# Optimization experiments

Measured on AMD Instinct MI355X. Metric: run time of the kernel, lower is better.

## Reference

```python
import jax, jax.numpy as jnp
import numpy as np

D_MODEL = 1024
N_HEADS = 16
HEAD_DIM = D_MODEL // N_HEADS
ROPE_BASE = 10000.0
RMS_EPS = 1e-5


def setup_inputs() -> dict:
    key = jax.random.key(0)
    k1, k2, k3 = jax.random.split(key, 3)
    B, T = 2, 2048
    x = jax.random.normal(k1, (B, T, D_MODEL), dtype=jnp.float32)
    norm_w = jnp.ones((D_MODEL,), dtype=jnp.float32)
    w_qkv = jax.random.normal(k2, (3 * D_MODEL, D_MODEL), dtype=jnp.float32) * (D_MODEL ** -0.5)
    w_out = jax.random.normal(k3, (D_MODEL, D_MODEL), dtype=jnp.float32) * (D_MODEL ** -0.5)
    return {"x": x, "norm_w": norm_w, "w_qkv": w_qkv, "w_out": w_out}


def _rope_cos_sin(T, dtype):
    inv_freq = 1.0 / (ROPE_BASE ** (jnp.arange(0, HEAD_DIM, 2, dtype=jnp.float32) / HEAD_DIM))
    t = jnp.arange(T, dtype=jnp.float32)
    freqs = t[:, None] * inv_freq[None, :]            # [T, HEAD_DIM//2]
    emb = jnp.concatenate([freqs, freqs], axis=-1)    # [T, HEAD_DIM]
    return jnp.cos(emb).astype(dtype), jnp.sin(emb).astype(dtype)


def _rotate_half(x):
    x1, x2 = jnp.split(x, 2, axis=-1)
    return jnp.concatenate([-x2, x1], axis=-1)


def reference(x, norm_w, w_qkv, w_out):
    B, T, _ = x.shape
    residual = x
    # RMSNorm
    rms = jax.lax.rsqrt(jnp.mean(x * x, axis=-1, keepdims=True) + RMS_EPS)
    xn = x * rms * norm_w
    # QKV projection (torch Linear: x @ W.T)
    qkv = xn @ w_qkv.T                                  # [B, T, 3*D]
    qkv = qkv.reshape(B, T, 3, N_HEADS, HEAD_DIM)
    q, k, v = qkv[:, :, 0], qkv[:, :, 1], qkv[:, :, 2]  # [B, T, H, hd]
    # RoPE on q, k
    cos, sin = _rope_cos_sin(T, q.dtype)                # [T, hd]
    cos = cos[None, :, None, :]
    sin = sin[None, :, None, :]
    q = q * cos + _rotate_half(q) * sin
    k = k * cos + _rotate_half(k) * sin
    # Bidirectional SDPA: [B, H, T, hd]
    qh = q.transpose(0, 2, 1, 3)
    kh = k.transpose(0, 2, 1, 3)
    vh = v.transpose(0, 2, 1, 3)
    scale = HEAD_DIM ** -0.5
    scores = jnp.einsum('bhqd,bhkd->bhqk', qh, kh) * scale
    attn = jax.nn.softmax(scores, axis=-1)
    out = jnp.einsum('bhqk,bhkd->bhqd', attn, vh)       # [B, H, T, hd]
    out = out.transpose(0, 2, 1, 3).reshape(B, T, D_MODEL)
    out = out @ w_out.T
    return residual + out
```

## Files before the change

kernel.cpp:

```cpp
#include <hip/hip_runtime.h>
#include <hip/hip_bf16.h>
#include <math.h>


typedef __bf16 bf16;
typedef __bf16 bf16x8 __attribute__((ext_vector_type(8)));
typedef __bf16 bf16x4 __attribute__((ext_vector_type(4)));
typedef float  f32x4  __attribute__((ext_vector_type(4)));
typedef unsigned u32x4 __attribute__((ext_vector_type(4)));

#define GLOAD16(g, l) __builtin_amdgcn_global_load_lds( \
    (const __attribute__((address_space(1))) void*)(g),  \
    (__attribute__((address_space(3))) void*)(l), 16, 0, 0)

__device__ __forceinline__ unsigned pk2(float a, float b) {
  unsigned short lo = __builtin_bit_cast(unsigned short, (bf16)a);
  unsigned short hi = __builtin_bit_cast(unsigned short, (bf16)b);
  return (unsigned)lo | ((unsigned)hi << 16);
}

__global__ __launch_bounds__(256) void k_cvt(const float* __restrict__ src,
    bf16* __restrict__ dst, int n) {
  int i = (blockIdx.x * 256 + threadIdx.x) * 8;
  if (i >= n) return;
  float4 a = *(const float4*)(src + i);
  float4 b = *(const float4*)(src + i + 4);
  bf16x8 o;
  o[0] = (bf16)a.x; o[1] = (bf16)a.y; o[2] = (bf16)a.z; o[3] = (bf16)a.w;
  o[4] = (bf16)b.x; o[5] = (bf16)b.y; o[6] = (bf16)b.z; o[7] = (bf16)b.w;
  *(bf16x8*)(dst + i) = o;
}

__global__ __launch_bounds__(256) void k_tab(float2* __restrict__ tab) {
  int idx = blockIdx.x * 256 + threadIdx.x;
  int t = idx >> 5, j = idx & 31;
  float invf = exp2f(-0.41524101186f * (float)j);
  float th = (float)t * invf;
  float sn, cs;
  sincosf(th, &sn, &cs);
  tab[idx] = make_float2(cs, sn);
}

__global__ __launch_bounds__(256) void k_rmsnorm(const float* __restrict__ x,
    const float* __restrict__ w, bf16* __restrict__ xn) {
  const int row = blockIdx.x, tid = threadIdx.x;
  float4 v = *(const float4*)(x + (size_t)row * 1024 + tid * 4);
  float ss = v.x * v.x + v.y * v.y + v.z * v.z + v.w * v.w;
  for (int m = 32; m >= 1; m >>= 1) ss += __shfl_xor(ss, m);
  __shared__ float red[4];
  if ((tid & 63) == 0) red[tid >> 6] = ss;
  __syncthreads();
  float ms = (red[0] + red[1] + red[2] + red[3]) * (1.f / 1024.f);
  float r = rsqrtf(ms + 1e-5f);
  float4 wv = *(const float4*)(w + tid * 4);
  bf16x4 o;
  o[0] = (bf16)(v.x * r * wv.x); o[1] = (bf16)(v.y * r * wv.y);
  o[2] = (bf16)(v.z * r * wv.z); o[3] = (bf16)(v.w * r * wv.w);
  *(bf16x4*)(xn + (size_t)row * 1024 + tid * 4) = o;
}

template<int RESID, int TM, int ROPE>
__global__ __launch_bounds__(256, (TM == 128) ? 3 : 2) void k_gemm_bt(
    const bf16* __restrict__ A, const bf16* __restrict__ B,
    const float* __restrict__ R, void* __restrict__ Cv,
    int M, int N, int K, int lda, const float2* __restrict__ tab) {
  constexpr int MT = TM / 32;
  constexpr int AELEM = TM * 64;
  constexpr int SMEM = (AELEM + 8192 > TM * 136) ? (AELEM + 8192) : (TM * 136);
  const int tid = threadIdx.x;
  const int lane = tid & 63, L15 = lane & 15, quad = lane >> 4;
  const int wave = tid >> 6, wr = wave >> 1, wc = wave & 1;
  const int n0 = blockIdx.x * 128, m0 = blockIdx.y * TM;
  __shared__ __align__(16) bf16 smem[SMEM];
  bf16* sA = smem; bf16* sB = smem + AELEM;
  f32x4 acc[MT][4];
  const f32x4 z = {0.f, 0.f, 0.f, 0.f};
  for (int i = 0; i < MT; i++) for (int j = 0; j < 4; j++) acc[i][j] = z;

  for (int k0 = 0; k0 < K; k0 += 64) {
    const bf16* Ab = A + (size_t)m0 * lda + k0;
    const bf16* Bb = B + (size_t)n0 * K + k0;
    for (int p = 0; p < TM / 32; p++) {
      int s = p * 256 + tid, r = s >> 3, c8 = (s & 7) ^ (r & 7);
      GLOAD16(Ab + (size_t)r * lda + c8 * 8, sA + s * 8);
    }
    for (int p = 0; p < 4; p++) {
      int s = p * 256 + tid, r = s >> 3, c8 = (s & 7) ^ (r & 7);
      GLOAD16(Bb + (size_t)r * K + c8 * 8, sB + s * 8);
    }
    __syncthreads();
    for (int kk = 0; kk < 2; kk++) {
      bf16x8 af[MT], bfv[4];
      for (int i = 0; i < MT; i++) {
        int ra = wr * (TM / 2) + i * 16 + L15;
        af[i] = *(const bf16x8*)(sA + ra * 64 + (((kk * 4 + quad) ^ (ra & 7)) * 8));
      }
      for (int i = 0; i < 4; i++) {
        int rb = wc * 64 + i * 16 + L15;
        bfv[i] = *(const bf16x8*)(sB + rb * 64 + (((kk * 4 + quad) ^ (rb & 7)) * 8));
      }
      __builtin_amdgcn_s_setprio(1);
      for (int mt = 0; mt < MT; mt++)
        for (int nt = 0; nt < 4; nt++)
          acc[mt][nt] = __builtin_amdgcn_mfma_f32_16x16x32_bf16(af[mt], bfv[nt], acc[mt][nt], 0, 0, 0);
      __builtin_amdgcn_s_setprio(0);
    }
    __syncthreads();
  }
  if (ROPE && (n0 >> 10) < 2) {
    const float qs = ((n0 >> 10) == 0) ? 0.18033688011f : 1.0f;
    const int tb = (m0 & 2047) + wr * (TM / 2);
    for (int mt = 0; mt < MT; mt++) {
      for (int nt = 0; nt < 2; nt++) {
        const int j = nt * 16 + L15;
        for (int g = 0; g < 4; g++) {
          int t = tb + mt * 16 + quad * 4 + g;
          float2 cs = tab[t * 32 + j];
          float lo = acc[mt][nt][g], hi = acc[mt][nt + 2][g];
          acc[mt][nt][g]     = (lo * cs.x - hi * cs.y) * qs;
          acc[mt][nt + 2][g] = (hi * cs.x + lo * cs.y) * qs;
        }
      }
    }
  }
  bf16* sC = smem;
  for (int mt = 0; mt < MT; mt++) for (int nt = 0; nt < 4; nt++) {
    int r = wr * (TM / 2) + mt * 16 + quad * 4, c = wc * 64 + nt * 16 + L15;
    f32x4 v = acc[mt][nt];
    for (int g = 0; g < 4; g++) sC[(r + g) * 136 + c] = (bf16)v[g];
  }
  __syncthreads();
  constexpr int TPR = 256 / TM;
  constexpr int CPT = 128 / TPR;
  const int rr = tid / TPR, sg = (tid % TPR) * CPT;
  const size_t row = (size_t)m0 + rr;
  const bf16* src = sC + rr * 136 + sg;
  if (RESID) {
    float* Cf = (float*)Cv;
    const float* rs = R + row * N + n0 + sg;
    float* dst = Cf + row * N + n0 + sg;
    for (int i = 0; i < CPT / 4; i++) {
      bf16x4 u = *(const bf16x4*)(src + i * 4);
      float4 rv = *(const float4*)(rs + i * 4);
      float4 o;
      o.x = (float)u[0] + rv.x; o.y = (float)u[1] + rv.y;
      o.z = (float)u[2] + rv.z; o.w = (float)u[3] + rv.w;
      *(float4*)(dst + i * 4) = o;
    }
  } else {
    bf16* Cb = (bf16*)Cv;
    bf16* dst = Cb + row * N + n0 + sg;
    for (int i = 0; i < CPT / 8; i++)
      *(bf16x8*)(dst + i * 8) = *(const bf16x8*)(src + i * 8);
  }
}

__global__ __launch_bounds__(256) void k_vt(const bf16* __restrict__ qkv,
    bf16* __restrict__ vt) {
  const int blk = blockIdx.x;
  const int tt = blk & 31, h = (blk >> 5) & 15, b = blk >> 9;
  const int tid = threadIdx.x;
  const int bh = b * 16 + h;
  __shared__ __align__(16) bf16 sT[64 * 72];
  for (int p = 0; p < 2; p++) {
    int s = p * 256 + tid, tl = s >> 3, c = s & 7;
    const bf16* vsrc = qkv + (size_t)(b * 2048 + tt * 64 + tl) * 3072 + 2048 + h * 64 + c * 8;
    *(bf16x8*)(sT + tl * 72 + c * 8) = *(const bf16x8*)vsrc;
  }
  __syncthreads();
  for (int p = 0; p < 2; p++) {
    int s = p * 256 + tid, d = s >> 3, tc = s & 7;
    bf16x8 v;
    for (int j = 0; j < 8; j++) v[j] = sT[(tc * 8 + j) * 72 + d];
    *(bf16x8*)(vt + (size_t)bh * 131072 + (size_t)d * 2048 + tt * 64 + tc * 8) = v;
  }
}

__global__ __launch_bounds__(256, 2) void k_attn(bf16* __restrict__ qkv,
    const bf16* __restrict__ vt) {
  const int tid = threadIdx.x;
  const int lane = tid & 63, L15 = lane & 15, quad = lane >> 4;
  const int wave = tid >> 6;
  const int bh = blockIdx.y, b = bh >> 4, h = bh & 15;
  const int q0 = blockIdx.x * 128;
  const bf16* Q  = qkv + (size_t)b * 2048 * 3072 + h * 64;
  const bf16* Kg = qkv + (size_t)b * 2048 * 3072 + 1024 + h * 64;
  const bf16* Vg = vt + (size_t)bh * 131072;
  __shared__ __align__(16) bf16 smem[32768];

  bf16x8 qf[2][2];
  for (int qt = 0; qt < 2; qt++) for (int kk = 0; kk < 2; kk++) {
    int rq = q0 + wave * 32 + qt * 16 + L15;
    qf[qt][kk] = *(const bf16x8*)(Q + (size_t)rq * 3072 + kk * 32 + quad * 8);
  }
  f32x4 o[4][2];
  const f32x4 z = {0.f, 0.f, 0.f, 0.f};
  for (int i = 0; i < 4; i++) for (int j = 0; j < 2; j++) o[i][j] = z;
  f32x4 o5[2] = {z, z};
  const bf16 one = (bf16)1.0f;
  const bf16x8 ones8 = {one, one, one, one, one, one, one, one};
  const float mcl = 7.21347602f;
  const f32x4 minit = {-mcl, -mcl, -mcl, -mcl};

  auto STAGE = [&](int kv0, int base) {
    const bf16* Kb = Kg + (size_t)kv0 * 3072;
    bf16* sKb = smem + base;
    bf16* sVb = smem + base + 8192;
    for (int p = 0; p < 4; p++) {
      int s = p * 256 + tid, r = s >> 3, c8 = (s & 7) ^ (r & 7);
      GLOAD16(Kb + (size_t)r * 3072 + c8 * 8, sKb + s * 8);
    }
    for (int p = 0; p < 4; p++) {
      int s = p * 256 + tid, r = s >> 4, cl = s & 15;
      int c8 = (cl & 8) | ((cl ^ (r & 7)) & 7);
      GLOAD16(Vg + (size_t)r * 2048 + kv0 + c8 * 8, sVb + s * 8);
    }
  };

  STAGE(0, 0);
  for (int t = 0; t < 16; ++t) {
    const int cur = (t & 1) << 14;
    if (t < 15) {
      STAGE((t + 1) << 7, cur ^ 16384);
      asm volatile("s_waitcnt vmcnt(8)" ::: "memory");
    } else {
      asm volatile("s_waitcnt vmcnt(0)" ::: "memory");
    }
    __builtin_amdgcn_s_barrier();
    __builtin_amdgcn_sched_barrier(0);
    const bf16* sK = smem + cur;
    const bf16* sV = smem + cur + 8192;

    f32x4 st[8][2];
    {
      bf16x8 kf[8];
#pragma unroll
      for (int kvt = 0; kvt < 8; kvt++) {
        int rk = kvt * 16 + L15;
        kf[kvt] = *(const bf16x8*)(sK + rk * 64 + ((quad ^ (rk & 7)) * 8));
      }
      __builtin_amdgcn_s_setprio(1);
#pragma unroll
      for (int kvt = 0; kvt < 8; kvt++)
        for (int qt = 0; qt < 2; qt++)
          st[kvt][qt] = __builtin_amdgcn_mfma_f32_16x16x32_bf16(kf[kvt], qf[qt][0], minit, 0, 0, 0);
      __builtin_amdgcn_s_setprio(0);
    }
    {
      bf16x8 kf[8];
#pragma unroll
      for (int kvt = 0; kvt < 8; kvt++) {
        int rk = kvt * 16 + L15;
        kf[kvt] = *(const bf16x8*)(sK + rk * 64 + (((4 + quad) ^ (rk & 7)) * 8));
      }
      __builtin_amdgcn_s_setprio(1);
#pragma unroll
      for (int kvt = 0; kvt < 8; kvt++)
        for (int qt = 0; qt < 2; qt++)
          st[kvt][qt] = __builtin_amdgcn_mfma_f32_16x16x32_bf16(kf[kvt], qf[qt][1], st[kvt][qt], 0, 0, 0);
      __builtin_amdgcn_s_setprio(0);
    }
    unsigned pA[2][8], pB[2][8];
#pragma unroll
    for (int qt = 0; qt < 2; qt++)
      for (int kvt = 0; kvt < 8; kvt++) {
        float p0 = __builtin_amdgcn_exp2f(st[kvt][qt][0]);
        float p1 = __builtin_amdgcn_exp2f(st[kvt][qt][1]);
        float p2 = __builtin_amdgcn_exp2f(st[kvt][qt][2]);
        float p3 = __builtin_amdgcn_exp2f(st[kvt][qt][3]);
        pA[qt][kvt] = pk2(p0, p1);
        pB[qt][kvt] = pk2(p2, p3);
      }
#pragma unroll
    for (int kc = 0; kc < 4; kc++) {
      bf16x8 vf[4];
#pragma unroll
      for (int dt = 0; dt < 4; dt++) {
        int rd = dt * 16 + L15;
        int c = kc * 4 + quad;
        int cs = (c & 8) | ((c ^ (rd & 7)) & 7);
        vf[dt] = *(const bf16x8*)(sV + rd * 128 + cs * 8);
      }
#pragma unroll
      for (int qt = 0; qt < 2; qt++) {
        auto rA = __builtin_amdgcn_permlane32_swap(pA[qt][2 * kc], pA[qt][2 * kc + 1], false, false);
        auto tAC = __builtin_amdgcn_permlane16_swap(rA[0], rA[1], false, false);
        auto rB = __builtin_amdgcn_permlane32_swap(pB[qt][2 * kc], pB[qt][2 * kc + 1], false, false);
        auto tBD = __builtin_amdgcn_permlane16_swap(rB[0], rB[1], false, false);
        u32x4 pw;
        pw[0] = tAC[0]; pw[1] = tBD[0]; pw[2] = tAC[1]; pw[3] = tBD[1];
        bf16x8 pf = __builtin_bit_cast(bf16x8, pw);
        __builtin_amdgcn_s_setprio(1);
#pragma unroll
        for (int dt = 0; dt < 4; dt++)
          o[dt][qt] = __builtin_amdgcn_mfma_f32_16x16x32_bf16(vf[dt], pf, o[dt][qt], 0, 0, 0);
        o5[qt] = __builtin_amdgcn_mfma_f32_16x16x32_bf16(ones8, pf, o5[qt], 0, 0, 0);
        __builtin_amdgcn_s_setprio(0);
      }
    }
    asm volatile("s_waitcnt lgkmcnt(0)" ::: "memory");
    __builtin_amdgcn_sched_barrier(0);
    __builtin_amdgcn_s_barrier();
  }
  float invl[2] = {1.f / o5[0][0], 1.f / o5[1][0]};
  bf16* sO = smem;
  for (int dt = 0; dt < 4; dt++) for (int qt = 0; qt < 2; qt++) {
    f32x4 v = o[dt][qt] * invl[qt];
    int ql = wave * 32 + qt * 16 + L15;
    uint2 w2; w2.x = pk2(v[0], v[1]); w2.y = pk2(v[2], v[3]);
    *(uint2*)(sO + ql * 72 + dt * 16 + quad * 4) = w2;
  }
  __syncthreads();
  const int rr = tid >> 1, sg = (tid & 1) * 32;
  const bf16* src = sO + rr * 72 + sg;
  bf16* dst = qkv + (size_t)(b * 2048 + q0 + rr) * 3072 + h * 64 + sg;
  for (int i = 0; i < 4; i++)
    *(bf16x8*)(dst + i * 8) = *(const bf16x8*)(src + i * 8);
}

extern "C" void kernel_launch(void* const* d_in, const int* in_sizes, int n_in,
                              void* d_out, int out_size, void* d_ws, size_t ws_size,
                              hipStream_t stream) {
  (void)in_sizes; (void)n_in; (void)out_size;
  const float* x     = (const float*)d_in[0];
  const float* normw = (const float*)d_in[1];
  const float* wqkv  = (const float*)d_in[2];
  const float* wout  = (const float*)d_in[3];
  float* out = (float*)d_out;
  bf16* ws  = (bf16*)d_ws;
  const size_t NQKV = (size_t)4096 * 3072, NXN = (size_t)4096 * 1024;
  const size_t NWQ = (size_t)3072 * 1024, NWO = (size_t)1024 * 1024;
  const size_t need = (NQKV + NXN + NWQ + NWO) * sizeof(bf16);
  if (ws_size < need) return;
  bf16* qkv    = ws;
  bf16* xn     = qkv + NQKV;
  bf16* vtp    = xn;
  bf16* wqkvb  = xn + NXN;
  bf16* woutb  = wqkvb + NWQ;
  float2* tab  = (float2*)out;
  k_cvt<<<(int)(NWQ / 8 / 256), 256, 0, stream>>>(wqkv, wqkvb, (int)NWQ);
  k_cvt<<<(int)(NWO / 8 / 256), 256, 0, stream>>>(wout, woutb, (int)NWO);
  k_tab<<<256, 256, 0, stream>>>(tab);
  k_rmsnorm<<<4096, 256, 0, stream>>>(x, normw, xn);
  k_gemm_bt<0, 128, 1><<<dim3(24, 32), 256, 0, stream>>>(xn, wqkvb, nullptr, qkv, 4096, 3072, 1024, 1024, tab);
  k_vt<<<1024, 256, 0, stream>>>(qkv, vtp);
  k_attn<<<dim3(16, 32), 256, 0, stream>>>(qkv, vtp);
  k_gemm_bt<1, 64, 0><<<dim3(8, 64), 256, 0, stream>>>(qkv, woutb, x, out, 4096, 1024, 1024, 3072, nullptr);
}
```

Baseline: 202.7 us.

## Split attention KV tile across two wave groups with shared-memory reduction

The attention kernel now runs 512 threads per block. Two groups of four waves each handle half of every 128-key tile for the same 128 queries, and the partial outputs and row sums are combined through shared memory at the end. The goal is more waves per block and less serial work per wave, which should improve latency hiding. The cost is an extra reduction step with shared-memory traffic and barriers, plus higher register and occupancy pressure from the 512,4 launch bounds.

Result: slower. 207.9 us (+2.6%).

```diff
diff --git a/kernel.cpp b/kernel.cpp
--- a/kernel.cpp
+++ b/kernel.cpp
@@ -176,11 +176,13 @@
   }
 }
 
-__global__ __launch_bounds__(256, 2) void k_attn(bf16* __restrict__ qkv,
+__global__ __launch_bounds__(512, 4) void k_attn(bf16* __restrict__ qkv,
     const bf16* __restrict__ vt) {
   const int tid = threadIdx.x;
   const int lane = tid & 63, L15 = lane & 15, quad = lane >> 4;
   const int wave = tid >> 6;
+  const int qw = wave & 3;
+  const int kvh = wave >> 2;
   const int bh = blockIdx.y, b = bh >> 4, h = bh & 15;
   const int q0 = blockIdx.x * 128;
   const bf16* Q  = qkv + (size_t)b * 2048 * 3072 + h * 64;
@@ -190,7 +192,7 @@
 
   bf16x8 qf[2][2];
   for (int qt = 0; qt < 2; qt++) for (int kk = 0; kk < 2; kk++) {
-    int rq = q0 + wave * 32 + qt * 16 + L15;
+    int rq = q0 + qw * 32 + qt * 16 + L15;
     qf[qt][kk] = *(const bf16x8*)(Q + (size_t)rq * 3072 + kk * 32 + quad * 8);
   }
   f32x4 o[4][2];
@@ -206,12 +208,12 @@
     const bf16* Kb = Kg + (size_t)kv0 * 3072;
     bf16* sKb = smem + base;
     bf16* sVb = smem + base + 8192;
-    for (int p = 0; p < 4; p++) {
-      int s = p * 256 + tid, r = s >> 3, c8 = (s & 7) ^ (r & 7);
+    for (int p = 0; p < 2; p++) {
+      int s = p * 512 + tid, r = s >> 3, c8 = (s & 7) ^ (r & 7);
       GLOAD16(Kb + (size_t)r * 3072 + c8 * 8, sKb + s * 8);
     }
-    for (int p = 0; p < 4; p++) {
-      int s = p * 256 + tid, r = s >> 4, cl = s & 15;
+    for (int p = 0; p < 2; p++) {
+      int s = p * 512 + tid, r = s >> 4, cl = s & 15;
       int c8 = (cl & 8) | ((cl ^ (r & 7)) & 7);
       GLOAD16(Vg + (size_t)r * 2048 + kv0 + c8 * 8, sVb + s * 8);
     }
@@ -222,7 +224,7 @@
     const int cur = (t & 1) << 14;
     if (t < 15) {
       STAGE((t + 1) << 7, cur ^ 16384);
-      asm volatile("s_waitcnt vmcnt(8)" ::: "memory");
+      asm volatile("s_waitcnt vmcnt(4)" ::: "memory");
     } else {
       asm volatile("s_waitcnt vmcnt(0)" ::: "memory");
     }
@@ -231,39 +233,39 @@
     const bf16* sK = smem + cur;
     const bf16* sV = smem + cur + 8192;
 
-    f32x4 st[8][2];
+    f32x4 st[4][2];
     {
-      bf16x8 kf[8];
-#pragma unroll
-      for (int kvt = 0; kvt < 8; kvt++) {
-        int rk = kvt * 16 + L15;
+      bf16x8 kf[4];
+#pragma unroll
+      for (int kvt = 0; kvt < 4; kvt++) {
+        int rk = kvh * 64 + kvt * 16 + L15;
         kf[kvt] = *(const bf16x8*)(sK + rk * 64 + ((quad ^ (rk & 7)) * 8));
       }
       __builtin_amdgcn_s_setprio(1);
 #pragma unroll
-      for (int kvt = 0; kvt < 8; kvt++)
+      for (int kvt = 0; kvt < 4; kvt++)
         for (int qt = 0; qt < 2; qt++)
           st[kvt][qt] = __builtin_amdgcn_mfma_f32_16x16x32_bf16(kf[kvt], qf[qt][0], minit, 0, 0, 0);
       __builtin_amdgcn_s_setprio(0);
     }
     {
-      bf16x8 kf[8];
-#pragma unroll
-      for (int kvt = 0; kvt < 8; kvt++) {
-        int rk = kvt * 16 + L15;
+      bf16x8 kf[4];
+#pragma unroll
+      for (int kvt = 0; kvt < 4; kvt++) {
+        int rk = kvh * 64 + kvt * 16 + L15;
         kf[kvt] = *(const bf16x8*)(sK + rk * 64 + (((4 + quad) ^ (rk & 7)) * 8));
       }
       __builtin_amdgcn_s_setprio(1);
 #pragma unroll
-      for (int kvt = 0; kvt < 8; kvt++)
+      for (int kvt = 0; kvt < 4; kvt++)
         for (int qt = 0; qt < 2; qt++)
           st[kvt][qt] = __builtin_amdgcn_mfma_f32_16x16x32_bf16(kf[kvt], qf[qt][1], st[kvt][qt], 0, 0, 0);
       __builtin_amdgcn_s_setprio(0);
     }
-    unsigned pA[2][8], pB[2][8];
+    unsigned pA[2][4], pB[2][4];
 #pragma unroll
     for (int qt = 0; qt < 2; qt++)
-      for (int kvt = 0; kvt < 8; kvt++) {
+      for (int kvt = 0; kvt < 4; kvt++) {
         float p0 = __builtin_amdgcn_exp2f(st[kvt][qt][0]);
         float p1 = __builtin_amdgcn_exp2f(st[kvt][qt][1]);
         float p2 = __builtin_amdgcn_exp2f(st[kvt][qt][2]);
@@ -272,12 +274,12 @@
         pB[qt][kvt] = pk2(p2, p3);
       }
 #pragma unroll
-    for (int kc = 0; kc < 4; kc++) {
+    for (int kc = 0; kc < 2; kc++) {
       bf16x8 vf[4];
 #pragma unroll
       for (int dt = 0; dt < 4; dt++) {
         int rd = dt * 16 + L15;
-        int c = kc * 4 + quad;
+        int c = kvh * 8 + kc * 4 + quad;
         int cs = (c & 8) | ((c ^ (rd & 7)) & 7);
         vf[dt] = *(const bf16x8*)(sV + rd * 128 + cs * 8);
       }
@@ -302,19 +304,36 @@
     __builtin_amdgcn_sched_barrier(0);
     __builtin_amdgcn_s_barrier();
   }
-  float invl[2] = {1.f / o5[0][0], 1.f / o5[1][0]};
-  bf16* sO = smem;
-  for (int dt = 0; dt < 4; dt++) for (int qt = 0; qt < 2; qt++) {
-    f32x4 v = o[dt][qt] * invl[qt];
-    int ql = wave * 32 + qt * 16 + L15;
-    uint2 w2; w2.x = pk2(v[0], v[1]); w2.y = pk2(v[2], v[3]);
-    *(uint2*)(sO + ql * 72 + dt * 16 + quad * 4) = w2;
-  }
-  __syncthreads();
-  const int rr = tid >> 1, sg = (tid & 1) * 32;
+  float* pO = (float*)smem;
+  float* pL = (float*)smem + 8704;
+  if (kvh == 1) {
+    for (int dt = 0; dt < 4; dt++) for (int qt = 0; qt < 2; qt++) {
+      int ql = qw * 32 + qt * 16 + L15;
+      *(f32x4*)(pO + (size_t)ql * 68 + dt * 16 + quad * 4) = o[dt][qt];
+    }
+    if (quad == 0)
+      for (int qt = 0; qt < 2; qt++)
+        pL[qw * 32 + qt * 16 + L15] = o5[qt][0];
+  }
+  __syncthreads();
+  bf16* sO = smem + 18432;
+  if (kvh == 0) {
+    float invl[2];
+    for (int qt = 0; qt < 2; qt++)
+      invl[qt] = 1.f / (o5[qt][0] + pL[qw * 32 + qt * 16 + L15]);
+    for (int dt = 0; dt < 4; dt++) for (int qt = 0; qt < 2; qt++) {
+      int ql = qw * 32 + qt * 16 + L15;
+      f32x4 part = *(const f32x4*)(pO + (size_t)ql * 68 + dt * 16 + quad * 4);
+      f32x4 v = (o[dt][qt] + part) * invl[qt];
+      uint2 w2; w2.x = pk2(v[0], v[1]); w2.y = pk2(v[2], v[3]);
+      *(uint2*)(sO + ql * 72 + dt * 16 + quad * 4) = w2;
+    }
+  }
+  __syncthreads();
+  const int rr = tid >> 2, sg = (tid & 3) * 16;
   const bf16* src = sO + rr * 72 + sg;
   bf16* dst = qkv + (size_t)(b * 2048 + q0 + rr) * 3072 + h * 64 + sg;
-  for (int i = 0; i < 4; i++)
+  for (int i = 0; i < 2; i++)
     *(bf16x8*)(dst + i * 8) = *(const bf16x8*)(src + i * 8);
 }
 
@@ -344,6 +363,6 @@
   k_rmsnorm<<<4096, 256, 0, stream>>>(x, normw, xn);
   k_gemm_bt<0, 128, 1><<<dim3(24, 32), 256, 0, stream>>>(xn, wqkvb, nullptr, qkv, 4096, 3072, 1024, 1024, tab);
   k_vt<<<1024, 256, 0, stream>>>(qkv, vtp);
-  k_attn<<<dim3(16, 32), 256, 0, stream>>>(qkv, vtp);
+  k_attn<<<dim3(16, 32), 512, 0, stream>>>(qkv, vtp);
   k_gemm_bt<1, 64, 0><<<dim3(8, 64), 256, 0, stream>>>(qkv, woutb, x, out, 4096, 1024, 1024, 3072, nullptr);
 }
```

## Merge prep kernels into one launch and interleave softmax exp with PV MFMAs

Applied to the files above, without the earlier changes.

Four preprocessing launches (two weight conversions, the RoPE table and RMSNorm) become a single k_prep kernel that picks its task by block index, removing three launch gaps. In the attention inner loop, the exp2 and bf16 packing of scores now happen per kc chunk, just before each group of PV MFMAs, instead of for the whole tile up front. This lowers the number of packed registers held at once and lets the exp work interleave with the MFMAs. The cost is more branching in the prep kernel and heavier reliance on the compiler's scheduling.

Measured after the change: 200.5 us. About the same (-1.1%).

```diff
diff --git a/kernel.cpp b/kernel.cpp
--- a/kernel.cpp
+++ b/kernel.cpp
@@ -19,31 +19,35 @@
   return (unsigned)lo | ((unsigned)hi << 16);
 }
 
-__global__ __launch_bounds__(256) void k_cvt(const float* __restrict__ src,
-    bf16* __restrict__ dst, int n) {
-  int i = (blockIdx.x * 256 + threadIdx.x) * 8;
-  if (i >= n) return;
-  float4 a = *(const float4*)(src + i);
-  float4 b = *(const float4*)(src + i + 4);
-  bf16x8 o;
-  o[0] = (bf16)a.x; o[1] = (bf16)a.y; o[2] = (bf16)a.z; o[3] = (bf16)a.w;
-  o[4] = (bf16)b.x; o[5] = (bf16)b.y; o[6] = (bf16)b.z; o[7] = (bf16)b.w;
-  *(bf16x8*)(dst + i) = o;
-}
-
-__global__ __launch_bounds__(256) void k_tab(float2* __restrict__ tab) {
-  int idx = blockIdx.x * 256 + threadIdx.x;
-  int t = idx >> 5, j = idx & 31;
-  float invf = exp2f(-0.41524101186f * (float)j);
-  float th = (float)t * invf;
-  float sn, cs;
-  sincosf(th, &sn, &cs);
-  tab[idx] = make_float2(cs, sn);
-}
-
-__global__ __launch_bounds__(256) void k_rmsnorm(const float* __restrict__ x,
-    const float* __restrict__ w, bf16* __restrict__ xn) {
-  const int row = blockIdx.x, tid = threadIdx.x;
+__global__ __launch_bounds__(256) void k_prep(
+    const float* __restrict__ wqkv, const float* __restrict__ wout,
+    const float* __restrict__ x, const float* __restrict__ w,
+    bf16* __restrict__ wqkvb, bf16* __restrict__ woutb,
+    bf16* __restrict__ xn, float2* __restrict__ tab) {
+  const int bid = blockIdx.x, tid = threadIdx.x;
+  if (bid < 2048) {
+    const float* src = (bid < 1536) ? wqkv : wout;
+    bf16* dst = (bid < 1536) ? wqkvb : woutb;
+    int i = ((bid < 1536 ? bid : bid - 1536) * 256 + tid) * 8;
+    float4 a = *(const float4*)(src + i);
+    float4 b = *(const float4*)(src + i + 4);
+    bf16x8 o;
+    o[0] = (bf16)a.x; o[1] = (bf16)a.y; o[2] = (bf16)a.z; o[3] = (bf16)a.w;
+    o[4] = (bf16)b.x; o[5] = (bf16)b.y; o[6] = (bf16)b.z; o[7] = (bf16)b.w;
+    *(bf16x8*)(dst + i) = o;
+    return;
+  }
+  if (bid < 2304) {
+    int idx = (bid - 2048) * 256 + tid;
+    int t = idx >> 5, j = idx & 31;
+    float invf = exp2f(-0.41524101186f * (float)j);
+    float th = (float)t * invf;
+    float sn, cs;
+    sincosf(th, &sn, &cs);
+    tab[idx] = make_float2(cs, sn);
+    return;
+  }
+  const int row = bid - 2304;
   float4 v = *(const float4*)(x + (size_t)row * 1024 + tid * 4);
   float ss = v.x * v.x + v.y * v.y + v.z * v.z + v.w * v.w;
   for (int m = 32; m >= 1; m >>= 1) ss += __shfl_xor(ss, m);
@@ -260,17 +264,6 @@
           st[kvt][qt] = __builtin_amdgcn_mfma_f32_16x16x32_bf16(kf[kvt], qf[qt][1], st[kvt][qt], 0, 0, 0);
       __builtin_amdgcn_s_setprio(0);
     }
-    unsigned pA[2][8], pB[2][8];
-#pragma unroll
-    for (int qt = 0; qt < 2; qt++)
-      for (int kvt = 0; kvt < 8; kvt++) {
-        float p0 = __builtin_amdgcn_exp2f(st[kvt][qt][0]);
-        float p1 = __builtin_amdgcn_exp2f(st[kvt][qt][1]);
-        float p2 = __builtin_amdgcn_exp2f(st[kvt][qt][2]);
-        float p3 = __builtin_amdgcn_exp2f(st[kvt][qt][3]);
-        pA[qt][kvt] = pk2(p0, p1);
-        pB[qt][kvt] = pk2(p2, p3);
-      }
 #pragma unroll
     for (int kc = 0; kc < 4; kc++) {
       bf16x8 vf[4];
@@ -281,11 +274,23 @@
         int cs = (c & 8) | ((c ^ (rd & 7)) & 7);
         vf[dt] = *(const bf16x8*)(sV + rd * 128 + cs * 8);
       }
+      unsigned pA[2][2], pB[2][2];
+#pragma unroll
+      for (int qt = 0; qt < 2; qt++)
+        for (int kq = 0; kq < 2; kq++) {
+          const f32x4 s4 = st[2 * kc + kq][qt];
+          float p0 = __builtin_amdgcn_exp2f(s4[0]);
+          float p1 = __builtin_amdgcn_exp2f(s4[1]);
+          float p2 = __builtin_amdgcn_exp2f(s4[2]);
+          float p3 = __builtin_amdgcn_exp2f(s4[3]);
+          pA[qt][kq] = pk2(p0, p1);
+          pB[qt][kq] = pk2(p2, p3);
+        }
 #pragma unroll
       for (int qt = 0; qt < 2; qt++) {
-        auto rA = __builtin_amdgcn_permlane32_swap(pA[qt][2 * kc], pA[qt][2 * kc + 1], false, false);
+        auto rA = __builtin_amdgcn_permlane32_swap(pA[qt][0], pA[qt][1], false, false);
         auto tAC = __builtin_amdgcn_permlane16_swap(rA[0], rA[1], false, false);
-        auto rB = __builtin_amdgcn_permlane32_swap(pB[qt][2 * kc], pB[qt][2 * kc + 1], false, false);
+        auto rB = __builtin_amdgcn_permlane32_swap(pB[qt][0], pB[qt][1], false, false);
         auto tBD = __builtin_amdgcn_permlane16_swap(rB[0], rB[1], false, false);
         u32x4 pw;
         pw[0] = tAC[0]; pw[1] = tBD[0]; pw[2] = tAC[1]; pw[3] = tBD[1];
@@ -338,10 +343,7 @@
   bf16* wqkvb  = xn + NXN;
   bf16* woutb  = wqkvb + NWQ;
   float2* tab  = (float2*)out;
-  k_cvt<<<(int)(NWQ / 8 / 256), 256, 0, stream>>>(wqkv, wqkvb, (int)NWQ);
-  k_cvt<<<(int)(NWO / 8 / 256), 256, 0, stream>>>(wout, woutb, (int)NWO);
-  k_tab<<<256, 256, 0, stream>>>(tab);
-  k_rmsnorm<<<4096, 256, 0, stream>>>(x, normw, xn);
+  k_prep<<<6400, 256, 0, stream>>>(wqkv, wout, x, normw, wqkvb, woutb, xn, tab);
   k_gemm_bt<0, 128, 1><<<dim3(24, 32), 256, 0, stream>>>(xn, wqkvb, nullptr, qkv, 4096, 3072, 1024, 1024, tab);
   k_vt<<<1024, 256, 0, stream>>>(qkv, vtp);
   k_attn<<<dim3(16, 32), 256, 0, stream>>>(qkv, vtp);
```
